# Kernel optimization log

Hardware: AMD Instinct MI355X
Metric: run time of the kernel (lower is better)

Reference implementation:

```python
import jax, jax.numpy as jnp
import numpy as np

N_IN, N_HID, N_OUT, T = 2048, 8192, 2048, 4096
DECAY, VTH, SURR_K = 0.9, 1.0, 4.0


def setup_inputs() -> dict:
    key = jax.random.key(0)
    k1, k2, k3 = jax.random.split(key, 3)
    input_stim = jax.random.uniform(k1, (1, N_IN, T), dtype=jnp.float32)
    W1 = jax.random.normal(k2, (N_HID, N_IN), dtype=jnp.float32) * np.float32(1.0 / np.sqrt(N_IN))
    W2 = jax.random.normal(k3, (N_OUT, N_HID), dtype=jnp.float32) * np.float32(1.0 / np.sqrt(N_HID))
    return {"input_stim": input_stim, "W1": W1, "W2": W2}


def _spike(v):
    # Hard threshold forward, sigmoid surrogate gradient backward.
    hard = (v >= VTH).astype(v.dtype)
    surr = jax.nn.sigmoid(SURR_K * (v - VTH))
    return surr + jax.lax.stop_gradient(hard - surr)


def reference(input_stim, W1, W2):
    # input_stim: [1, N_IN, T]; loop starts at t=1 as in the source.
    x_seq = jnp.swapaxes(input_stim[0, :, 1:], 0, 1)  # [T-1, N_IN]
    v1_0 = jnp.zeros((N_HID,), dtype=input_stim.dtype)
    v2_0 = jnp.zeros((N_OUT,), dtype=input_stim.dtype)

    def step(carry, x_t):
        v1, v2 = carry
        v1 = v1 * DECAY + W1 @ x_t          # synapse 0 post input + leaky integrate
        s1 = _spike(v1)
        v1 = v1 * (1.0 - s1)                # reset spiked neurons
        v2 = v2 * DECAY + W2 @ s1           # synapse 1 post input + leaky integrate
        s2 = _spike(v2)
        v2 = v2 * (1.0 - s2)
        return (v1, v2), (s1, s2)

    _, (S1, S2) = jax.lax.scan(step, (v1_0, v2_0), x_seq)
    # spike_times layout in source: [n_neurons, T-1]
    return S1.T, S2.T
```

## Files before the change

kernel.cpp:

```cpp
#include <hip/hip_runtime.h>


#define HN 8192
#define NI 2048
#define NO 2048
#define TFULL 4096
#define NTS 4095
#define CS 512

__device__ float g_v1[HN];
__device__ float g_v2[NO];
__device__ float g_Xt[(size_t)CS * NI];
__device__ float g_C1[(size_t)HN * CS];
__device__ float g_S1t[(size_t)CS * HN];
__device__ float g_C2[(size_t)NO * CS];

__global__ void zero_state() {
    int i = blockIdx.x * 256 + threadIdx.x;
    if (i < HN) g_v1[i] = 0.0f;
    if (i < NO) g_v2[i] = 0.0f;
}

__global__ void sentinel_kernel(float* __restrict__ out, size_t n) {
    size_t i = (size_t)blockIdx.x * 256 + threadIdx.x;
    if (i < n) out[i] = 16.0f;
}

__global__ void transpose_x(const float* __restrict__ X, int t0, int tc) {
    __shared__ float tile[32][33];
    int tbase = blockIdx.x * 32;
    int kbase = blockIdx.y * 32;
    int lx = threadIdx.x, ly = threadIdx.y;
#pragma unroll
    for (int r = 0; r < 4; ++r) {
        int k = kbase + ly + 8 * r;
        int t = tbase + lx;
        float v = 0.0f;
        if (t < tc) v = X[(size_t)k * TFULL + 1 + t0 + t];
        tile[ly + 8 * r][lx] = v;
    }
    __syncthreads();
#pragma unroll
    for (int r = 0; r < 4; ++r) {
        int t = tbase + ly + 8 * r;
        int k = kbase + lx;
        g_Xt[(size_t)t * NI + k] = tile[lx][ly + 8 * r];
    }
}

__device__ __forceinline__ int swzf(int g, int e, int h) {
    int b = (((g * 64 + e) * 32) + h * 16) ^ (((e >> 2) & 7) << 4);
    return b >> 2;
}

__device__ __forceinline__ void gemm_body(const float* __restrict__ A, int lda,
                                          const float* __restrict__ B, int ldb,
                                          float* __restrict__ C, int KTOT) {
    __shared__ float As[4096];
    __shared__ float Bs[4096];
    const int tid = threadIdx.x;
    const int tm = tid & 15;
    const int tt = tid >> 4;
    const int m0 = blockIdx.y * 64;
    const int t0 = blockIdx.x * 64;
    const int lr = tid >> 4;
    const int lc = tid & 15;

    float acc[4][4][8];
    float y[4][4];
#pragma unroll
    for (int i = 0; i < 4; ++i)
#pragma unroll
        for (int s = 0; s < 4; ++s) {
#pragma unroll
            for (int j = 0; j < 8; ++j) acc[i][s][j] = 0.0f;
        }

    for (int kt = 0; kt < KTOT; kt += 64) {
        __syncthreads();
#pragma unroll
        for (int it = 0; it < 4; ++it) {
            int rr = lr + it * 16;
            float4 v = *(const float4*)&A[(size_t)(m0 + rr) * lda + kt + lc * 4];
            *(float4*)&As[swzf(lc >> 1, rr, lc & 1)] = v;
        }
#pragma unroll
        for (int it = 0; it < 4; ++it) {
            int rr = lr + it * 16;
            float4 v = *(const float4*)&B[(size_t)(t0 + rr) * ldb + kt + lc * 4];
            *(float4*)&Bs[swzf(lc >> 1, rr, lc & 1)] = v;
        }
        __syncthreads();
#pragma unroll
        for (int g = 0; g < 8; ++g) {
#pragma unroll
            for (int hf = 0; hf < 2; ++hf) {
                float a[4][4], b[4][4];
#pragma unroll
                for (int i = 0; i < 4; ++i)
                    *(float4*)a[i] = *(const float4*)&As[swzf(g, tm * 4 + i, hf)];
#pragma unroll
                for (int s = 0; s < 4; ++s)
                    *(float4*)b[s] = *(const float4*)&Bs[swzf(g, tt * 4 + s, hf)];
#pragma unroll
                for (int i = 0; i < 4; ++i)
#pragma unroll
                    for (int s = 0; s < 4; ++s)
#pragma unroll
                        for (int j = 0; j < 4; ++j)
                            acc[i][s][hf * 4 + j] =
                                fmaf(a[i][j], b[s][j], acc[i][s][hf * 4 + j]);
            }
        }
        if (((kt + 64) & 2047) == 0) {
            bool first = (kt + 64) == 2048;
#pragma unroll
            for (int i = 0; i < 4; ++i)
#pragma unroll
                for (int s = 0; s < 4; ++s) {
                    float* u = acc[i][s];
                    float s0 = __fadd_rn(u[0], u[4]);
                    float s1 = __fadd_rn(u[1], u[5]);
                    float s2 = __fadd_rn(u[2], u[6]);
                    float s3 = __fadd_rn(u[3], u[7]);
                    float d = __fadd_rn(__fadd_rn(s0, s1), __fadd_rn(s2, s3));
                    y[i][s] = first ? d : __fadd_rn(y[i][s], d);
#pragma unroll
                    for (int j = 0; j < 8; ++j) u[j] = 0.0f;
                }
        }
    }
#pragma unroll
    for (int i = 0; i < 4; ++i) {
        int m = m0 + tm * 4 + i;
#pragma unroll
        for (int s = 0; s < 4; ++s) {
            int t = t0 + tt * 4 + s;
            C[(size_t)m * CS + t] = y[i][s];
        }
    }
}

__global__ __launch_bounds__(256)
void gemm1(const float* __restrict__ W1) {
    gemm_body(W1, NI, g_Xt, NI, g_C1, NI);
}

__global__ __launch_bounds__(256)
void gemm2(const float* __restrict__ W2) {
    gemm_body(W2, HN, g_S1t, HN, g_C2, HN);
}

__global__ void scan1(float* __restrict__ S1o, int t0, int tc) {
    int h = blockIdx.x * 256 + threadIdx.x;
    float v = g_v1[h];
    const float* c = g_C1 + (size_t)h * CS;
    float* so = S1o + (size_t)h * NTS + t0;
    for (int t = 0; t < CS; ++t) {
        if (t < tc) {
            v = __fadd_rn(__fmul_rn(v, 0.9f), c[t]);
            float s = 0.0f;
            if (v >= 1.0f) { s = 1.0f; v = 0.0f; }
            so[t] = s;
            g_S1t[(size_t)t * HN + h] = s;
        } else {
            g_S1t[(size_t)t * HN + h] = 0.0f;
        }
    }
    g_v1[h] = v;
}

__global__ void scan2(float* __restrict__ S2o, int t0, int tc) {
    int o = blockIdx.x * 256 + threadIdx.x;
    float v = g_v2[o];
    const float* c = g_C2 + (size_t)o * CS;
    float* so = S2o + (size_t)o * NTS + t0;
    for (int t = 0; t < tc; ++t) {
        v = __fadd_rn(__fmul_rn(v, 0.9f), c[t]);
        float s = 0.0f;
        if (v >= 1.0f) { s = 1.0f; v = 0.0f; }
        so[t] = s;
    }
    g_v2[o] = v;
}

extern "C" void kernel_launch(void* const* d_in, const int* in_sizes, int n_in,
                              void* d_out, int out_size, void* d_ws, size_t ws_size,
                              hipStream_t stream) {
    (void)d_ws; (void)ws_size;
    float* out = (float*)d_out;

    bool ok = (n_in == 3)
           && (in_sizes[0] == NI * TFULL)
           && (in_sizes[1] == HN * NI)
           && (in_sizes[2] == NO * HN)
           && (out_size == (HN + NO) * NTS);
    if (!ok) {
        size_t n = (size_t)(HN + NO) * NTS;
        sentinel_kernel<<<(int)((n + 255) / 256), 256, 0, stream>>>(out, n);
        return;
    }

    const float* X  = (const float*)d_in[0];
    const float* W1 = (const float*)d_in[1];
    const float* W2 = (const float*)d_in[2];

    float* S1o = out;
    float* S2o = out + (size_t)HN * NTS;

    zero_state<<<(HN + 255) / 256, 256, 0, stream>>>();

    for (int t0 = 0; t0 < NTS; t0 += CS) {
        int tc = NTS - t0; if (tc > CS) tc = CS;

        transpose_x<<<dim3(CS / 32, NI / 32), dim3(32, 8), 0, stream>>>(X, t0, tc);

        gemm1<<<dim3(CS / 64, HN / 64), 256, 0, stream>>>(W1);

        scan1<<<HN / 256, 256, 0, stream>>>(S1o, t0, tc);

        gemm2<<<dim3(CS / 64, NO / 64), 256, 0, stream>>>(W2);

        scan2<<<NO / 256, 256, 0, stream>>>(S2o, t0, tc);
    }
}
```

Baseline: 17.12 ms.

## Halve GEMM N-tile, prefetch next K-tile into registers, vectorize scan loads

The GEMM tile shrinks from 64x64 to 64x32, doubling the block count for better occupancy, and the global loads for the next K-slice are prefetched into registers while the current slice is being computed. KTOT becomes a template parameter. The scan kernels now read the input currents as float4 and unroll by four. The aim is to hide global memory latency and use more of the GPU, at the cost of less data reuse per block.

```diff
diff --git a/kernel.cpp b/kernel.cpp
--- a/kernel.cpp
+++ b/kernel.cpp
@@ -48,64 +48,81 @@
     }
 }
 
-__device__ __forceinline__ int swzf(int g, int e, int h) {
-    int b = (((g * 64 + e) * 32) + h * 16) ^ (((e >> 2) & 7) << 4);
+__device__ __forceinline__ int swzA(int g, int e, int h) {
+    int b = (((g << 6) + e) << 5) + (h << 4);
+    b ^= ((e >> 2) & 7) << 4;
     return b >> 2;
 }
-
+__device__ __forceinline__ int swzB(int g, int e, int h) {
+    int b = (((g << 5) + e) << 5) + (h << 4);
+    b ^= ((e >> 2) & 7) << 4;
+    return b >> 2;
+}
+
+template <int KTOT>
 __device__ __forceinline__ void gemm_body(const float* __restrict__ A, int lda,
                                           const float* __restrict__ B, int ldb,
-                                          float* __restrict__ C, int KTOT) {
+                                          float* __restrict__ C) {
     __shared__ float As[4096];
-    __shared__ float Bs[4096];
+    __shared__ float Bs[2048];
     const int tid = threadIdx.x;
     const int tm = tid & 15;
     const int tt = tid >> 4;
     const int m0 = blockIdx.y * 64;
-    const int t0 = blockIdx.x * 64;
+    const int t0 = blockIdx.x * 32;
     const int lr = tid >> 4;
-    const int lc = tid & 15;
-
-    float acc[4][4][8];
-    float y[4][4];
+    const int kq = tid & 15;
+    const int lg = kq >> 1, lh = kq & 1;
+
+    float acc[4][2][8];
+    float y[4][2];
 #pragma unroll
     for (int i = 0; i < 4; ++i)
 #pragma unroll
-        for (int s = 0; s < 4; ++s) {
+        for (int s = 0; s < 2; ++s)
 #pragma unroll
             for (int j = 0; j < 8; ++j) acc[i][s][j] = 0.0f;
-        }
+
+    float4 ra[4], rb[2];
+#pragma unroll
+    for (int it = 0; it < 4; ++it)
+        ra[it] = *(const float4*)&A[(size_t)(m0 + lr + it * 16) * lda + kq * 4];
+#pragma unroll
+    for (int it = 0; it < 2; ++it)
+        rb[it] = *(const float4*)&B[(size_t)(t0 + lr + it * 16) * ldb + kq * 4];
 
     for (int kt = 0; kt < KTOT; kt += 64) {
         __syncthreads();
 #pragma unroll
-        for (int it = 0; it < 4; ++it) {
-            int rr = lr + it * 16;
-            float4 v = *(const float4*)&A[(size_t)(m0 + rr) * lda + kt + lc * 4];
-            *(float4*)&As[swzf(lc >> 1, rr, lc & 1)] = v;
-        }
-#pragma unroll
-        for (int it = 0; it < 4; ++it) {
-            int rr = lr + it * 16;
-            float4 v = *(const float4*)&B[(size_t)(t0 + rr) * ldb + kt + lc * 4];
-            *(float4*)&Bs[swzf(lc >> 1, rr, lc & 1)] = v;
-        }
+        for (int it = 0; it < 4; ++it)
+            *(float4*)&As[swzA(lg, lr + it * 16, lh)] = ra[it];
+#pragma unroll
+        for (int it = 0; it < 2; ++it)
+            *(float4*)&Bs[swzB(lg, lr + it * 16, lh)] = rb[it];
         __syncthreads();
+        if (kt + 64 < KTOT) {
+#pragma unroll
+            for (int it = 0; it < 4; ++it)
+                ra[it] = *(const float4*)&A[(size_t)(m0 + lr + it * 16) * lda + kt + 64 + kq * 4];
+#pragma unroll
+            for (int it = 0; it < 2; ++it)
+                rb[it] = *(const float4*)&B[(size_t)(t0 + lr + it * 16) * ldb + kt + 64 + kq * 4];
+        }
 #pragma unroll
         for (int g = 0; g < 8; ++g) {
 #pragma unroll
             for (int hf = 0; hf < 2; ++hf) {
-                float a[4][4], b[4][4];
+                float a[4][4], b[2][4];
 #pragma unroll
                 for (int i = 0; i < 4; ++i)
-                    *(float4*)a[i] = *(const float4*)&As[swzf(g, tm * 4 + i, hf)];
-#pragma unroll
-                for (int s = 0; s < 4; ++s)
-                    *(float4*)b[s] = *(const float4*)&Bs[swzf(g, tt * 4 + s, hf)];
+                    *(float4*)a[i] = *(const float4*)&As[swzA(g, tm * 4 + i, hf)];
+#pragma unroll
+                for (int s = 0; s < 2; ++s)
+                    *(float4*)b[s] = *(const float4*)&Bs[swzB(g, tt * 2 + s, hf)];
 #pragma unroll
                 for (int i = 0; i < 4; ++i)
 #pragma unroll
-                    for (int s = 0; s < 4; ++s)
+                    for (int s = 0; s < 2; ++s)
 #pragma unroll
                         for (int j = 0; j < 4; ++j)
                             acc[i][s][hf * 4 + j] =
@@ -117,7 +134,7 @@
 #pragma unroll
             for (int i = 0; i < 4; ++i)
 #pragma unroll
-                for (int s = 0; s < 4; ++s) {
+                for (int s = 0; s < 2; ++s) {
                     float* u = acc[i][s];
                     float s0 = __fadd_rn(u[0], u[4]);
                     float s1 = __fadd_rn(u[1], u[5]);
@@ -134,21 +151,19 @@
     for (int i = 0; i < 4; ++i) {
         int m = m0 + tm * 4 + i;
 #pragma unroll
-        for (int s = 0; s < 4; ++s) {
-            int t = t0 + tt * 4 + s;
-            C[(size_t)m * CS + t] = y[i][s];
-        }
+        for (int s = 0; s < 2; ++s)
+            C[(size_t)m * CS + t0 + tt * 2 + s] = y[i][s];
     }
 }
 
 __global__ __launch_bounds__(256)
 void gemm1(const float* __restrict__ W1) {
-    gemm_body(W1, NI, g_Xt, NI, g_C1, NI);
+    gemm_body<NI>(W1, NI, g_Xt, NI, g_C1);
 }
 
 __global__ __launch_bounds__(256)
 void gemm2(const float* __restrict__ W2) {
-    gemm_body(W2, HN, g_S1t, HN, g_C2, HN);
+    gemm_body<HN>(W2, HN, g_S1t, HN, g_C2);
 }
 
 __global__ void scan1(float* __restrict__ S1o, int t0, int tc) {
@@ -156,15 +171,21 @@
     float v = g_v1[h];
     const float* c = g_C1 + (size_t)h * CS;
     float* so = S1o + (size_t)h * NTS + t0;
-    for (int t = 0; t < CS; ++t) {
-        if (t < tc) {
-            v = __fadd_rn(__fmul_rn(v, 0.9f), c[t]);
-            float s = 0.0f;
-            if (v >= 1.0f) { s = 1.0f; v = 0.0f; }
-            so[t] = s;
-            g_S1t[(size_t)t * HN + h] = s;
-        } else {
-            g_S1t[(size_t)t * HN + h] = 0.0f;
+    for (int t = 0; t < CS; t += 4) {
+        float4 c4 = *(const float4*)&c[t];
+        float cc[4] = {c4.x, c4.y, c4.z, c4.w};
+#pragma unroll
+        for (int q = 0; q < 4; ++q) {
+            int tt = t + q;
+            if (tt < tc) {
+                v = __fadd_rn(__fmul_rn(v, 0.9f), cc[q]);
+                float s = 0.0f;
+                if (v >= 1.0f) { s = 1.0f; v = 0.0f; }
+                so[tt] = s;
+                g_S1t[(size_t)tt * HN + h] = s;
+            } else {
+                g_S1t[(size_t)tt * HN + h] = 0.0f;
+            }
         }
     }
     g_v1[h] = v;
@@ -175,11 +196,19 @@
     float v = g_v2[o];
     const float* c = g_C2 + (size_t)o * CS;
     float* so = S2o + (size_t)o * NTS + t0;
-    for (int t = 0; t < tc; ++t) {
-        v = __fadd_rn(__fmul_rn(v, 0.9f), c[t]);
-        float s = 0.0f;
-        if (v >= 1.0f) { s = 1.0f; v = 0.0f; }
-        so[t] = s;
+    for (int t = 0; t < CS; t += 4) {
+        float4 c4 = *(const float4*)&c[t];
+        float cc[4] = {c4.x, c4.y, c4.z, c4.w};
+#pragma unroll
+        for (int q = 0; q < 4; ++q) {
+            int tt = t + q;
+            if (tt < tc) {
+                v = __fadd_rn(__fmul_rn(v, 0.9f), cc[q]);
+                float s = 0.0f;
+                if (v >= 1.0f) { s = 1.0f; v = 0.0f; }
+                so[tt] = s;
+            }
+        }
     }
     g_v2[o] = v;
 }
@@ -215,11 +244,11 @@
 
         transpose_x<<<dim3(CS / 32, NI / 32), dim3(32, 8), 0, stream>>>(X, t0, tc);
 
-        gemm1<<<dim3(CS / 64, HN / 64), 256, 0, stream>>>(W1);
+        gemm1<<<dim3(CS / 32, HN / 64), 256, 0, stream>>>(W1);
 
         scan1<<<HN / 256, 256, 0, stream>>>(S1o, t0, tc);
 
-        gemm2<<<dim3(CS / 64, NO / 64), 256, 0, stream>>>(W2);
+        gemm2<<<dim3(CS / 32, NO / 64), 256, 0, stream>>>(W2);
 
         scan2<<<NO / 256, 256, 0, stream>>>(S2o, t0, tc);
     }
```

After: 14.83 ms. -13.4%, faster.
